# Performance work log

Measured on AMD Instinct MI355X. Metric: run time of the kernel, lower is better.

Reference implementation:

```python
import jax, jax.numpy as jnp
import numpy as np

B, L, H, W, C = 2, 5, 48, 176, 256
HEADS, DIM_HEAD = 8, 32
INNER = HEADS * DIM_HEAD  # 256
SCALE = DIM_HEAD ** -0.5


def setup_inputs() -> dict:
    key = jax.random.key(0)
    k1, k2, k3, k4, k5 = jax.random.split(key, 5)
    x = jax.random.normal(k1, (B, L, H, W, C), dtype=jnp.float32)
    # mask of shape (B, H, W, 1, L); slot 0 always valid so no softmax row is fully masked
    mask = jax.random.randint(k2, (B, H, W, 1, L), 0, 2, dtype=jnp.int32)
    mask = mask.at[..., 0].set(1)
    w_qkv = jax.random.normal(k3, (C, 3 * INNER), dtype=jnp.float32) / np.sqrt(C)
    w_out = jax.random.normal(k4, (INNER, C), dtype=jnp.float32) / np.sqrt(INNER)
    b_out = jax.random.normal(k5, (C,), dtype=jnp.float32) * 0.01
    return {"x": x, "mask": mask, "w_qkv": w_qkv, "w_out": w_out, "b_out": b_out}


def reference(x, mask, w_qkv, w_out, b_out):
    # x: (B, L, H, W, C) -> (B, H, W, L, C)
    xp = jnp.transpose(x, (0, 2, 3, 1, 4))
    qkv = xp @ w_qkv  # (B, H, W, L, 3*INNER)
    q, k, v = jnp.split(qkv, 3, axis=-1)
    # split heads: (B, H, W, L, M, D)
    shp = (B, H, W, L, HEADS, DIM_HEAD)
    q = q.reshape(shp)
    k = k.reshape(shp)
    v = v.reshape(shp)
    # attention over the small CAV axis L
    att = jnp.einsum('bhwimd,bhwjmd->bmhwij', q, k) * SCALE  # (B,M,H,W,L,L)
    m = mask[:, None]  # (B,1,H,W,1,L) broadcasts over (B,M,H,W,i,j)
    att = jnp.where(m == 0, -jnp.inf, att)
    att = jax.nn.softmax(att, axis=-1)
    out = jnp.einsum('bmhwij,bhwjmd->bhwimd', att, v)  # (B,H,W,L,M,D)
    out = out.reshape(B, H, W, L, INNER)
    out = out @ w_out + b_out  # dropout is identity in eval
    return jnp.transpose(out, (0, 3, 1, 2, 4))  # (B, L, H, W, C)
```

## Files before the change

### kernel.cpp

```cpp
#include <hip/hip_runtime.h>


typedef __attribute__((ext_vector_type(8))) short short8;
typedef __attribute__((ext_vector_type(4))) float f32x4;

#define SCALE_F 0.17677669529663687f

static __device__ __forceinline__ float b2f(unsigned short u) {
    union { unsigned u; float f; } x; x.u = ((unsigned)u) << 16; return x.f;
}
static __device__ __forceinline__ unsigned short f2b(float f) {
    union { float f; unsigned u; } x; x.f = f;
    unsigned u = x.u;
    return (unsigned short)((u + 0x7FFFu + ((u >> 16) & 1u)) >> 16);
}

static __device__ __forceinline__ size_t row_to_xoff(int r) {
    int l = r % 5; int t = r / 5;
    int w = t % 176; t /= 176;
    int h = t % 48; int b = t / 48;
    return (size_t)(((b * 5 + l) * 48 + h) * 176 + w) * 256;
}

static __device__ __forceinline__ int lidx(int r, int c) {
    return r * 256 + ((((c >> 3) ^ (r & 7)) << 3) | (c & 7));
}

static __device__ __forceinline__ void async_cp16(const unsigned short* g, unsigned short* l) {
    __builtin_amdgcn_global_load_lds(
        (__attribute__((address_space(1))) void*)(void*)g,
        (__attribute__((address_space(3))) void*)(void*)l, 16, 0, 0);
}

static __device__ __forceinline__ void barrier_lgkm() {
    __builtin_amdgcn_s_waitcnt(0xC07F);
    __builtin_amdgcn_s_barrier();
}

__global__ __launch_bounds__(256) void k_prep(const float* __restrict__ wq,
                                              const float* __restrict__ wo,
                                              unsigned short* __restrict__ wqt,
                                              unsigned short* __restrict__ wot) {
    int i = blockIdx.x * 256 + threadIdx.x;
    if (i < 196608) { int k = i / 768, n = i % 768; wqt[n * 256 + k] = f2b(wq[i]); }
    if (i < 65536)  { int k = i / 256, n = i % 256; wot[n * 256 + k] = f2b(wo[i]); }
}

template<int C>
static __device__ __forceinline__ void issue_chunk(const unsigned short* __restrict__ wqt,
                                                   const unsigned short* __restrict__ wot,
                                                   unsigned short* __restrict__ Bw,
                                                   int n0w, int lane) {
    constexpr int p = C >> 3;
    constexpr int kk = C & 7;
    constexpr int slot = C & 1;
    const unsigned short* wbase = (p < 3) ? (wqt + p * 65536) : wot;
#pragma unroll
    for (int t = 0; t < 2; ++t) {
        int cidx = t * 64 + lane;
        int nl = cidx >> 2;
        int kq = (cidx & 3) ^ ((nl >> 1) & 3);
        const unsigned short* g = wbase + (n0w + nl) * 256 + kk * 32 + kq * 8;
        async_cp16(g, Bw + slot * 1024 + t * 512);
    }
}

template<int C>
static __device__ __forceinline__ void chunk_step(f32x4 (&acc)[5][2],
        const unsigned short* __restrict__ As, unsigned short* __restrict__ Bw,
        const unsigned short* __restrict__ wqt, const unsigned short* __restrict__ wot,
        int n0w, int lane) {
    constexpr int kk = C & 7;
    constexpr int slot = C & 1;
    constexpr int imm = (C == 31) ? 0xF70 : 0xF72;
    const int ln = lane & 15, quad = lane >> 4;
    __builtin_amdgcn_s_waitcnt(imm);
    short8 b[2];
#pragma unroll
    for (int n = 0; n < 2; ++n)
        b[n] = *(const short8*)&Bw[slot * 1024 + (n * 16 + ln) * 32
                                   + ((quad ^ ((ln >> 1) & 3)) * 8)];
    __builtin_amdgcn_s_waitcnt(0xC07F);
    if constexpr (C + 2 < 32) issue_chunk<C + 2>(wqt, wot, Bw, n0w, lane);
    short8 a[5];
#pragma unroll
    for (int m = 0; m < 5; ++m)
        a[m] = *(const short8*)&As[lidx(m * 16 + ln, kk * 32 + quad * 8)];
#pragma unroll
    for (int m = 0; m < 5; ++m)
#pragma unroll
        for (int n = 0; n < 2; ++n)
            acc[m][n] = __builtin_amdgcn_mfma_f32_16x16x32_bf16(a[m], b[n], acc[m][n], 0, 0, 0);
}

template<int P>
static __device__ __forceinline__ void gemm8(f32x4 (&acc)[5][2],
        const unsigned short* __restrict__ As, unsigned short* __restrict__ Bw,
        const unsigned short* __restrict__ wqt, const unsigned short* __restrict__ wot,
        int n0w, int lane) {
    chunk_step<P * 8 + 0>(acc, As, Bw, wqt, wot, n0w, lane);
    chunk_step<P * 8 + 1>(acc, As, Bw, wqt, wot, n0w, lane);
    chunk_step<P * 8 + 2>(acc, As, Bw, wqt, wot, n0w, lane);
    chunk_step<P * 8 + 3>(acc, As, Bw, wqt, wot, n0w, lane);
    chunk_step<P * 8 + 4>(acc, As, Bw, wqt, wot, n0w, lane);
    chunk_step<P * 8 + 5>(acc, As, Bw, wqt, wot, n0w, lane);
    chunk_step<P * 8 + 6>(acc, As, Bw, wqt, wot, n0w, lane);
    chunk_step<P * 8 + 7>(acc, As, Bw, wqt, wot, n0w, lane);
}

static __device__ __forceinline__ void cstore(const f32x4 (&acc)[5][2],
        unsigned short* __restrict__ Ds, int n0w, int lane) {
    const int ln = lane & 15, quad = lane >> 4;
#pragma unroll
    for (int m = 0; m < 5; ++m)
#pragma unroll
        for (int n = 0; n < 2; ++n)
#pragma unroll
            for (int rg = 0; rg < 4; ++rg)
                Ds[lidx(m * 16 + quad * 4 + rg, n0w + n * 16 + ln)] = f2b(acc[m][n][rg]);
}

__global__ __launch_bounds__(512, 2) void k_fused(const float* __restrict__ x,
                                                  const int* __restrict__ mask,
                                                  const unsigned short* __restrict__ wqt,
                                                  const unsigned short* __restrict__ wot,
                                                  const float* __restrict__ bo,
                                                  float* __restrict__ out) {
    __shared__ __align__(16) unsigned short xs[80 * 256];
    __shared__ __align__(16) unsigned short qs[80 * 256];
    __shared__ __align__(16) unsigned short kvs[80 * 256];
    __shared__ __align__(16) unsigned short Bb[8 * 2048];

    const int tid = threadIdx.x;
    const int blk = blockIdx.x;
    const int rbase = blk * 80;
    const int lane = tid & 63, wv = tid >> 6;
    const int n0w = wv * 32;
    unsigned short* Bw = Bb + wv * 2048;

#pragma unroll
    for (int i = 0; i < 5; ++i) {
        int u = i * 512 + tid;
        int r = u >> 5, cb = u & 31;
        size_t xo = row_to_xoff(rbase + r) + cb * 8;
        float4 v0 = *(const float4*)(x + xo);
        float4 v1 = *(const float4*)(x + xo + 4);
        short8 o;
        o[0] = (short)f2b(v0.x); o[1] = (short)f2b(v0.y);
        o[2] = (short)f2b(v0.z); o[3] = (short)f2b(v0.w);
        o[4] = (short)f2b(v1.x); o[5] = (short)f2b(v1.y);
        o[6] = (short)f2b(v1.z); o[7] = (short)f2b(v1.w);
        *(short8*)&xs[lidx(r, cb * 8)] = o;
    }

    const int part = tid & 3, hh = (tid >> 2) & 7, g = tid >> 5;
    int mk[5];
#pragma unroll
    for (int j = 0; j < 5; ++j) mk[j] = mask[(blk * 16 + g) * 5 + j];

    issue_chunk<0>(wqt, wot, Bw, n0w, lane);
    issue_chunk<1>(wqt, wot, Bw, n0w, lane);

    barrier_lgkm();

    {
        f32x4 acc[5][2];
#pragma unroll
        for (int m = 0; m < 5; ++m)
#pragma unroll
            for (int n = 0; n < 2; ++n) acc[m][n] = (f32x4){0.f, 0.f, 0.f, 0.f};
        gemm8<0>(acc, xs, Bw, wqt, wot, n0w, lane);
        cstore(acc, qs, n0w, lane);
    }
    {
        f32x4 acc[5][2];
#pragma unroll
        for (int m = 0; m < 5; ++m)
#pragma unroll
            for (int n = 0; n < 2; ++n) acc[m][n] = (f32x4){0.f, 0.f, 0.f, 0.f};
        gemm8<1>(acc, xs, Bw, wqt, wot, n0w, lane);
        cstore(acc, kvs, n0w, lane);
    }
    barrier_lgkm();

    float pr[5][5];
    {
        const int c0 = hh * 32 + part * 8;
        float qf[5][8];
#pragma unroll
        for (int i = 0; i < 5; ++i) {
            short8 qv = *(const short8*)&qs[lidx(g * 5 + i, c0)];
#pragma unroll
            for (int d = 0; d < 8; ++d) qf[i][d] = b2f((unsigned short)qv[d]);
        }
        float s[5][5];
#pragma unroll
        for (int j = 0; j < 5; ++j) {
            short8 kv = *(const short8*)&kvs[lidx(g * 5 + j, c0)];
            float kf[8];
#pragma unroll
            for (int d = 0; d < 8; ++d) kf[d] = b2f((unsigned short)kv[d]);
#pragma unroll
            for (int i = 0; i < 5; ++i) {
                float acc = 0.f;
#pragma unroll
                for (int d = 0; d < 8; ++d) acc += qf[i][d] * kf[d];
                s[i][j] = acc;
            }
        }
#pragma unroll
        for (int i = 0; i < 5; ++i)
#pragma unroll
            for (int j = 0; j < 5; ++j) {
                s[i][j] += __shfl_xor(s[i][j], 1, 64);
                s[i][j] += __shfl_xor(s[i][j], 2, 64);
            }
#pragma unroll
        for (int i = 0; i < 5; ++i) {
            float mx = -1e30f;
#pragma unroll
            for (int j = 0; j < 5; ++j) {
                s[i][j] = mk[j] ? s[i][j] * SCALE_F : -1e30f;
                mx = fmaxf(mx, s[i][j]);
            }
            float sum = 0.f;
#pragma unroll
            for (int j = 0; j < 5; ++j) { pr[i][j] = __expf(s[i][j] - mx); sum += pr[i][j]; }
            float inv = 1.f / sum;
#pragma unroll
            for (int j = 0; j < 5; ++j) pr[i][j] *= inv;
        }
    }
    barrier_lgkm();

    {
        f32x4 acc[5][2];
#pragma unroll
        for (int m = 0; m < 5; ++m)
#pragma unroll
            for (int n = 0; n < 2; ++n) acc[m][n] = (f32x4){0.f, 0.f, 0.f, 0.f};
        gemm8<2>(acc, xs, Bw, wqt, wot, n0w, lane);
        cstore(acc, kvs, n0w, lane);
    }
    barrier_lgkm();

    {
        const int c0 = hh * 32 + part * 8;
        float o[5][8];
#pragma unroll
        for (int i = 0; i < 5; ++i)
#pragma unroll
            for (int d = 0; d < 8; ++d) o[i][d] = 0.f;
#pragma unroll
        for (int j = 0; j < 5; ++j) {
            short8 vv = *(const short8*)&kvs[lidx(g * 5 + j, c0)];
            float vf[8];
#pragma unroll
            for (int d = 0; d < 8; ++d) vf[d] = b2f((unsigned short)vv[d]);
#pragma unroll
            for (int i = 0; i < 5; ++i)
#pragma unroll
                for (int d = 0; d < 8; ++d) o[i][d] += pr[i][j] * vf[d];
        }
#pragma unroll
        for (int i = 0; i < 5; ++i) {
            short8 ov;
#pragma unroll
            for (int d = 0; d < 8; ++d) ov[d] = (short)f2b(o[i][d]);
            *(short8*)&kvs[lidx(g * 5 + i, c0)] = ov;
        }
    }
    barrier_lgkm();

    {
        f32x4 acc[5][2];
#pragma unroll
        for (int m = 0; m < 5; ++m)
#pragma unroll
            for (int n = 0; n < 2; ++n) acc[m][n] = (f32x4){0.f, 0.f, 0.f, 0.f};
        gemm8<3>(acc, kvs, Bw, wqt, wot, n0w, lane);
        const int ln = lane & 15, quad = lane >> 4;
        float bv[2];
#pragma unroll
        for (int n = 0; n < 2; ++n) bv[n] = bo[n0w + n * 16 + ln];
#pragma unroll
        for (int m = 0; m < 5; ++m)
#pragma unroll
            for (int rg = 0; rg < 4; ++rg) {
                int row = m * 16 + quad * 4 + rg;
                size_t off = row_to_xoff(rbase + row);
#pragma unroll
                for (int n = 0; n < 2; ++n)
                    out[off + n0w + n * 16 + ln] = acc[m][n][rg] + bv[n];
            }
    }
}

extern "C" void kernel_launch(void* const* d_in, const int* in_sizes, int n_in,
                              void* d_out, int out_size, void* d_ws, size_t ws_size,
                              hipStream_t stream) {
    const float* x   = (const float*)d_in[0];
    const int* mask  = (const int*)d_in[1];
    const float* wq  = (const float*)d_in[2];
    const float* wo  = (const float*)d_in[3];
    const float* bo  = (const float*)d_in[4];
    float* out = (float*)d_out;

    char* ws = (char*)d_ws;
    unsigned short* wqt = (unsigned short*)(ws);
    unsigned short* wot = (unsigned short*)(ws + 393216);

    hipLaunchKernelGGL(k_prep, dim3(768), dim3(256), 0, stream, wq, wo, wqt, wot);
    hipLaunchKernelGGL(k_fused, dim3(1056), dim3(512), 0, stream, x, mask, wqt, wot, bo, out);
}
```

Measured before the change: 243.6 us.

## Load weights directly from global into registers and fuse Q/K/V GEMMs

Removes the per-wave LDS double-buffered async weight staging and instead loads the B fragments straight from global memory (L2-resident) into registers. The Q, K and V projections are computed in one k-loop sharing A-fragment loads, with V accumulators held in registers across the softmax phase. The weight prep kernel becomes a tiled LDS transpose with coalesced reads and writes. This trades LDS traffic and shared memory footprint for higher register pressure (60 accumulator vectors live) and exposed global-load latency in the MFMA loop.

```diff
diff --git a/kernel.cpp b/kernel.cpp
--- a/kernel.cpp
+++ b/kernel.cpp
@@ -26,12 +26,6 @@
     return r * 256 + ((((c >> 3) ^ (r & 7)) << 3) | (c & 7));
 }
 
-static __device__ __forceinline__ void async_cp16(const unsigned short* g, unsigned short* l) {
-    __builtin_amdgcn_global_load_lds(
-        (__attribute__((address_space(1))) void*)(void*)g,
-        (__attribute__((address_space(3))) void*)(void*)l, 16, 0, 0);
-}
-
 static __device__ __forceinline__ void barrier_lgkm() {
     __builtin_amdgcn_s_waitcnt(0xC07F);
     __builtin_amdgcn_s_barrier();
@@ -41,71 +35,30 @@
                                               const float* __restrict__ wo,
                                               unsigned short* __restrict__ wqt,
                                               unsigned short* __restrict__ wot) {
-    int i = blockIdx.x * 256 + threadIdx.x;
-    if (i < 196608) { int k = i / 768, n = i % 768; wqt[n * 256 + k] = f2b(wq[i]); }
-    if (i < 65536)  { int k = i / 256, n = i % 256; wot[n * 256 + k] = f2b(wo[i]); }
-}
-
-template<int C>
-static __device__ __forceinline__ void issue_chunk(const unsigned short* __restrict__ wqt,
-                                                   const unsigned short* __restrict__ wot,
-                                                   unsigned short* __restrict__ Bw,
-                                                   int n0w, int lane) {
-    constexpr int p = C >> 3;
-    constexpr int kk = C & 7;
-    constexpr int slot = C & 1;
-    const unsigned short* wbase = (p < 3) ? (wqt + p * 65536) : wot;
-#pragma unroll
-    for (int t = 0; t < 2; ++t) {
-        int cidx = t * 64 + lane;
-        int nl = cidx >> 2;
-        int kq = (cidx & 3) ^ ((nl >> 1) & 3);
-        const unsigned short* g = wbase + (n0w + nl) * 256 + kk * 32 + kq * 8;
-        async_cp16(g, Bw + slot * 1024 + t * 512);
-    }
-}
-
-template<int C>
-static __device__ __forceinline__ void chunk_step(f32x4 (&acc)[5][2],
-        const unsigned short* __restrict__ As, unsigned short* __restrict__ Bw,
-        const unsigned short* __restrict__ wqt, const unsigned short* __restrict__ wot,
-        int n0w, int lane) {
-    constexpr int kk = C & 7;
-    constexpr int slot = C & 1;
-    constexpr int imm = (C == 31) ? 0xF70 : 0xF72;
-    const int ln = lane & 15, quad = lane >> 4;
-    __builtin_amdgcn_s_waitcnt(imm);
-    short8 b[2];
-#pragma unroll
-    for (int n = 0; n < 2; ++n)
-        b[n] = *(const short8*)&Bw[slot * 1024 + (n * 16 + ln) * 32
-                                   + ((quad ^ ((ln >> 1) & 3)) * 8)];
-    __builtin_amdgcn_s_waitcnt(0xC07F);
-    if constexpr (C + 2 < 32) issue_chunk<C + 2>(wqt, wot, Bw, n0w, lane);
-    short8 a[5];
-#pragma unroll
-    for (int m = 0; m < 5; ++m)
-        a[m] = *(const short8*)&As[lidx(m * 16 + ln, kk * 32 + quad * 8)];
-#pragma unroll
-    for (int m = 0; m < 5; ++m)
-#pragma unroll
-        for (int n = 0; n < 2; ++n)
-            acc[m][n] = __builtin_amdgcn_mfma_f32_16x16x32_bf16(a[m], b[n], acc[m][n], 0, 0, 0);
-}
-
-template<int P>
-static __device__ __forceinline__ void gemm8(f32x4 (&acc)[5][2],
-        const unsigned short* __restrict__ As, unsigned short* __restrict__ Bw,
-        const unsigned short* __restrict__ wqt, const unsigned short* __restrict__ wot,
-        int n0w, int lane) {
-    chunk_step<P * 8 + 0>(acc, As, Bw, wqt, wot, n0w, lane);
-    chunk_step<P * 8 + 1>(acc, As, Bw, wqt, wot, n0w, lane);
-    chunk_step<P * 8 + 2>(acc, As, Bw, wqt, wot, n0w, lane);
-    chunk_step<P * 8 + 3>(acc, As, Bw, wqt, wot, n0w, lane);
-    chunk_step<P * 8 + 4>(acc, As, Bw, wqt, wot, n0w, lane);
-    chunk_step<P * 8 + 5>(acc, As, Bw, wqt, wot, n0w, lane);
-    chunk_step<P * 8 + 6>(acc, As, Bw, wqt, wot, n0w, lane);
-    chunk_step<P * 8 + 7>(acc, As, Bw, wqt, wot, n0w, lane);
+    __shared__ unsigned short tile[64 * 65];
+    const int bb = blockIdx.x;
+    const float* src; unsigned short* dst; int kt, nt, ncols;
+    if (bb < 48) { kt = bb / 12; nt = bb % 12; src = wq; dst = wqt; ncols = 768; }
+    else { int b2 = bb - 48; kt = b2 >> 2; nt = b2 & 3; src = wo; dst = wot; ncols = 256; }
+    const int t = threadIdx.x;
+#pragma unroll
+    for (int p = 0; p < 4; ++p) {
+        int u = p * 256 + t; int r = u >> 4, c4 = u & 15;
+        float4 v = *(const float4*)&src[(size_t)(kt * 64 + r) * ncols + nt * 64 + c4 * 4];
+        tile[r * 65 + c4 * 4 + 0] = f2b(v.x);
+        tile[r * 65 + c4 * 4 + 1] = f2b(v.y);
+        tile[r * 65 + c4 * 4 + 2] = f2b(v.z);
+        tile[r * 65 + c4 * 4 + 3] = f2b(v.w);
+    }
+    __syncthreads();
+#pragma unroll
+    for (int p = 0; p < 2; ++p) {
+        int u = p * 256 + t; int n = u >> 3, c8 = u & 7;
+        short8 o;
+#pragma unroll
+        for (int j = 0; j < 8; ++j) o[j] = (short)tile[(c8 * 8 + j) * 65 + n];
+        *(short8*)&dst[(nt * 64 + n) * 256 + kt * 64 + c8 * 8] = o;
+    }
 }
 
 static __device__ __forceinline__ void cstore(const f32x4 (&acc)[5][2],
@@ -129,14 +82,13 @@
     __shared__ __align__(16) unsigned short xs[80 * 256];
     __shared__ __align__(16) unsigned short qs[80 * 256];
     __shared__ __align__(16) unsigned short kvs[80 * 256];
-    __shared__ __align__(16) unsigned short Bb[8 * 2048];
 
     const int tid = threadIdx.x;
     const int blk = blockIdx.x;
     const int rbase = blk * 80;
     const int lane = tid & 63, wv = tid >> 6;
     const int n0w = wv * 32;
-    unsigned short* Bw = Bb + wv * 2048;
+    const int ln = lane & 15, quad = lane >> 4;
 
 #pragma unroll
     for (int i = 0; i < 5; ++i) {
@@ -158,29 +110,52 @@
 #pragma unroll
     for (int j = 0; j < 5; ++j) mk[j] = mask[(blk * 16 + g) * 5 + j];
 
-    issue_chunk<0>(wqt, wot, Bw, n0w, lane);
-    issue_chunk<1>(wqt, wot, Bw, n0w, lane);
-
-    barrier_lgkm();
-
-    {
-        f32x4 acc[5][2];
-#pragma unroll
-        for (int m = 0; m < 5; ++m)
-#pragma unroll
-            for (int n = 0; n < 2; ++n) acc[m][n] = (f32x4){0.f, 0.f, 0.f, 0.f};
-        gemm8<0>(acc, xs, Bw, wqt, wot, n0w, lane);
-        cstore(acc, qs, n0w, lane);
-    }
-    {
-        f32x4 acc[5][2];
-#pragma unroll
-        for (int m = 0; m < 5; ++m)
-#pragma unroll
-            for (int n = 0; n < 2; ++n) acc[m][n] = (f32x4){0.f, 0.f, 0.f, 0.f};
-        gemm8<1>(acc, xs, Bw, wqt, wot, n0w, lane);
-        cstore(acc, kvs, n0w, lane);
-    }
+    const unsigned short* wq_l = wqt + (n0w + ln) * 256 + quad * 8;
+    const unsigned short* wo_l = wot + (n0w + ln) * 256 + quad * 8;
+
+    barrier_lgkm();
+
+    f32x4 aq[5][2], ak[5][2], av[5][2];
+#pragma unroll
+    for (int m = 0; m < 5; ++m)
+#pragma unroll
+        for (int n = 0; n < 2; ++n) {
+            aq[m][n] = (f32x4){0.f, 0.f, 0.f, 0.f};
+            ak[m][n] = (f32x4){0.f, 0.f, 0.f, 0.f};
+            av[m][n] = (f32x4){0.f, 0.f, 0.f, 0.f};
+        }
+#pragma unroll
+    for (int kk = 0; kk < 8; ++kk) {
+        short8 a[5];
+#pragma unroll
+        for (int m = 0; m < 5; ++m)
+            a[m] = *(const short8*)&xs[lidx(m * 16 + ln, kk * 32 + quad * 8)];
+        short8 bq[2], bk[2], bv[2];
+#pragma unroll
+        for (int n = 0; n < 2; ++n) {
+            int o = n * (16 * 256) + kk * 32;
+            bq[n] = *(const short8*)&wq_l[o];
+            bk[n] = *(const short8*)&wq_l[o + 256 * 256];
+            bv[n] = *(const short8*)&wq_l[o + 512 * 256];
+        }
+#pragma unroll
+        for (int m = 0; m < 5; ++m)
+#pragma unroll
+            for (int n = 0; n < 2; ++n)
+                aq[m][n] = __builtin_amdgcn_mfma_f32_16x16x32_bf16(a[m], bq[n], aq[m][n], 0, 0, 0);
+#pragma unroll
+        for (int m = 0; m < 5; ++m)
+#pragma unroll
+            for (int n = 0; n < 2; ++n)
+                ak[m][n] = __builtin_amdgcn_mfma_f32_16x16x32_bf16(a[m], bk[n], ak[m][n], 0, 0, 0);
+#pragma unroll
+        for (int m = 0; m < 5; ++m)
+#pragma unroll
+            for (int n = 0; n < 2; ++n)
+                av[m][n] = __builtin_amdgcn_mfma_f32_16x16x32_bf16(a[m], bv[n], av[m][n], 0, 0, 0);
+    }
+    cstore(aq, qs, n0w, lane);
+    cstore(ak, kvs, n0w, lane);
     barrier_lgkm();
 
     float pr[5][5];
@@ -233,15 +208,7 @@
     }
     barrier_lgkm();
 
-    {
-        f32x4 acc[5][2];
-#pragma unroll
-        for (int m = 0; m < 5; ++m)
-#pragma unroll
-            for (int n = 0; n < 2; ++n) acc[m][n] = (f32x4){0.f, 0.f, 0.f, 0.f};
-        gemm8<2>(acc, xs, Bw, wqt, wot, n0w, lane);
-        cstore(acc, kvs, n0w, lane);
-    }
+    cstore(av, kvs, n0w, lane);
     barrier_lgkm();
 
     {
@@ -273,16 +240,30 @@
     barrier_lgkm();
 
     {
-        f32x4 acc[5][2];
-#pragma unroll
-        for (int m = 0; m < 5; ++m)
-#pragma unroll
-            for (int n = 0; n < 2; ++n) acc[m][n] = (f32x4){0.f, 0.f, 0.f, 0.f};
-        gemm8<3>(acc, kvs, Bw, wqt, wot, n0w, lane);
-        const int ln = lane & 15, quad = lane >> 4;
-        float bv[2];
-#pragma unroll
-        for (int n = 0; n < 2; ++n) bv[n] = bo[n0w + n * 16 + ln];
+        f32x4 ao[5][2];
+#pragma unroll
+        for (int m = 0; m < 5; ++m)
+#pragma unroll
+            for (int n = 0; n < 2; ++n) ao[m][n] = (f32x4){0.f, 0.f, 0.f, 0.f};
+#pragma unroll
+        for (int kk = 0; kk < 8; ++kk) {
+            short8 a[5];
+#pragma unroll
+            for (int m = 0; m < 5; ++m)
+                a[m] = *(const short8*)&kvs[lidx(m * 16 + ln, kk * 32 + quad * 8)];
+            short8 bn[2];
+#pragma unroll
+            for (int n = 0; n < 2; ++n)
+                bn[n] = *(const short8*)&wo_l[n * (16 * 256) + kk * 32];
+#pragma unroll
+            for (int m = 0; m < 5; ++m)
+#pragma unroll
+                for (int n = 0; n < 2; ++n)
+                    ao[m][n] = __builtin_amdgcn_mfma_f32_16x16x32_bf16(a[m], bn[n], ao[m][n], 0, 0, 0);
+        }
+        float bv2[2];
+#pragma unroll
+        for (int n = 0; n < 2; ++n) bv2[n] = bo[n0w + n * 16 + ln];
 #pragma unroll
         for (int m = 0; m < 5; ++m)
 #pragma unroll
@@ -291,7 +272,7 @@
                 size_t off = row_to_xoff(rbase + row);
 #pragma unroll
                 for (int n = 0; n < 2; ++n)
-                    out[off + n0w + n * 16 + ln] = acc[m][n][rg] + bv[n];
+                    out[off + n0w + n * 16 + ln] = ao[m][n][rg] + bv2[n];
             }
     }
 }
@@ -310,6 +291,6 @@
     unsigned short* wqt = (unsigned short*)(ws);
     unsigned short* wot = (unsigned short*)(ws + 393216);
 
-    hipLaunchKernelGGL(k_prep, dim3(768), dim3(256), 0, stream, wq, wo, wqt, wot);
+    hipLaunchKernelGGL(k_prep, dim3(64), dim3(256), 0, stream, wq, wo, wqt, wot);
     hipLaunchKernelGGL(k_fused, dim3(1056), dim3(512), 0, stream, x, mask, wqt, wot, bo, out);
 }
```

New measurement: 267.8 us. +9.9%, slower.
